# Kernel tuning notes

Hardware: AMD Instinct MI355X
Metric: run time of the kernel (lower is better)

The kernel has to match this reference:

```python
import jax, jax.numpy as jnp
import numpy as np

EPS = 1e-09


def make_spd(x):
    # x: [B1, B2, n, n] random normal -> SPD via Gram matrix + jitter
    n = x.shape[-1]
    g = jnp.einsum('...ik,...jk->...ij', x, x) / n
    return g + 1e-3 * jnp.eye(n, dtype=x.dtype)


def setup_inputs() -> dict:
    key = jax.random.key(0)
    x = jax.random.normal(key, (256, 32, 64, 64), dtype=jnp.float32)
    return {"inputs": make_spd(x)}


def reference(inputs) -> jnp.ndarray:
    # Batched matrix log of SPD matrices: V @ diag(log(relu(w)+eps)) @ V^T
    eigval, eigvecs = jnp.linalg.eigh(inputs)            # [..., n], [..., n, n]
    log_s = jnp.log(jax.nn.relu(eigval) + EPS)           # [..., n]
    # fused reconstruction: (V * log_s) @ V^T
    return jnp.einsum('...ij,...j,...kj->...ik', eigvecs, log_s, eigvecs)
```

## Files before the change

kernel.cpp:

```cpp
#include <hip/hip_runtime.h>
#include <math.h>

#define NDIM 64
#define PITCH 68
#define MAXSWEEPS 20

__global__ __launch_bounds__(64, 2)
void logeig_jacobi_kernel(const float* __restrict__ in, float* __restrict__ out)
{
    const int b    = blockIdx.x;
    const int lane = threadIdx.x;
    const float* A = in  + (size_t)b * (NDIM * NDIM);
    float*       O = out + (size_t)b * (NDIM * NDIM);

    __shared__ float lds[NDIM * PITCH + NDIM];

    float x[NDIM];
#pragma unroll
    for (int i = 0; i < NDIM; ++i)
        x[i] = A[i * NDIM + lane];

    float alpha = 0.0f;
#pragma unroll
    for (int i = 0; i < NDIM; ++i) alpha = fmaf(x[i], x[i], alpha);

#pragma unroll 1
    for (int sweep = 0; sweep < MAXSWEEPS; ++sweep) {
        float a2 = 0.0f;
#pragma unroll
        for (int i = 0; i < NDIM; ++i) a2 = fmaf(x[i], x[i], a2);
        alpha = a2;

        bool sweep_rot = false;
#pragma unroll 1
        for (int mi = 1; mi < NDIM; ++mi) {
            const int m    = (sweep & 1) ? (NDIM - mi) : mi;
            const int pidx = (lane ^ m) << 2;

            float y[NDIM];
#pragma unroll
            for (int i = 0; i < NDIM; ++i)
                y[i] = __int_as_float(__builtin_amdgcn_ds_bpermute(pidx, __float_as_int(x[i])));

            float gamma = 0.0f;
#pragma unroll
            for (int i = 0; i < NDIM; ++i) gamma = fmaf(x[i], y[i], gamma);

            const float other = __int_as_float(__builtin_amdgcn_ds_bpermute(pidx, __float_as_int(alpha)));

            const bool  is_p = lane < (lane ^ m);
            const float aa = is_p ? alpha : other;
            const float bb = is_p ? other : alpha;

            const bool big = (gamma * gamma) > (1e-12f * aa * bb);
            if (__ballot(big) != 0ull) sweep_rot = true;

            const bool rot = (gamma != 0.0f);
            float zeta = (bb - aa) / (2.0f * gamma);
            float az   = fabsf(zeta);
            float t    = 1.0f / (az + sqrtf(1.0f + az * az));
            t = (zeta < 0.0f) ? -t : t;
            float cc = 1.0f / sqrtf(1.0f + t * t);
            float ss = t * cc;

            const float sgn = is_p ? -1.0f : 1.0f;
            const float c_r = rot ? cc : 1.0f;
            const float s_r = rot ? sgn * ss : 0.0f;
            const float tg  = rot ? sgn * t * gamma : 0.0f;

#pragma unroll
            for (int i = 0; i < NDIM; ++i)
                x[i] = fmaf(c_r, x[i], s_r * y[i]);
            alpha += tg;
        }
        if (!sweep_rot) break;
    }

    float af = 0.0f;
#pragma unroll
    for (int i = 0; i < NDIM; ++i) af = fmaf(x[i], x[i], af);
    const float lam = sqrtf(af);
    const float w   = logf(lam + 1e-9f) / af;

    float4* row = (float4*)&lds[lane * PITCH];
#pragma unroll
    for (int t4 = 0; t4 < NDIM / 4; ++t4)
        row[t4] = make_float4(x[4 * t4 + 0], x[4 * t4 + 1], x[4 * t4 + 2], x[4 * t4 + 3]);
    lds[NDIM * PITCH + lane] = w;
    __syncthreads();

    float acc[NDIM];
#pragma unroll
    for (int i = 0; i < NDIM; ++i) acc[i] = 0.0f;

#pragma unroll 1
    for (int k = 0; k < NDIM; ++k) {
        const float wk  = lds[NDIM * PITCH + k];
        const float mjk = lds[k * PITCH + lane];
        const float zk  = wk * mjk;
        const float4* rowk = (const float4*)&lds[k * PITCH];
#pragma unroll
        for (int t4 = 0; t4 < NDIM / 4; ++t4) {
            const float4 v = rowk[t4];
            acc[4 * t4 + 0] = fmaf(zk, v.x, acc[4 * t4 + 0]);
            acc[4 * t4 + 1] = fmaf(zk, v.y, acc[4 * t4 + 1]);
            acc[4 * t4 + 2] = fmaf(zk, v.z, acc[4 * t4 + 2]);
            acc[4 * t4 + 3] = fmaf(zk, v.w, acc[4 * t4 + 3]);
        }
    }

#pragma unroll
    for (int i = 0; i < NDIM; ++i)
        O[i * NDIM + lane] = acc[i];
}

extern "C" void kernel_launch(void* const* d_in, const int* in_sizes, int n_in,
                              void* d_out, int out_size, void* d_ws, size_t ws_size,
                              hipStream_t stream)
{
    const float* in  = (const float*)d_in[0];
    float*       out = (float*)d_out;
    const int nmat = out_size / (NDIM * NDIM);
    hipLaunchKernelGGL(logeig_jacobi_kernel, dim3(nmat), dim3(64), 0, stream, in, out);
}
```

Baseline: 5.825 ms.

## Loosen Jacobi convergence, split dot-product accumulators, chunk LDS reconstruction, raise occupancy

Relaxes the off-diagonal convergence threshold so sweeps can terminate earlier, and splits the gamma dot product into four independent accumulators to shorten the dependency chain. It also stages eigenvector rows into a smaller 16-row LDS buffer in chunks to cut shared memory, and raises the launch-bounds occupancy hint. The looser tolerance risks slightly less accurate eigen-decompositions, and the chunking adds extra barriers.

```diff
diff --git a/kernel.cpp b/kernel.cpp
--- a/kernel.cpp
+++ b/kernel.cpp
@@ -3,9 +3,10 @@
 
 #define NDIM 64
 #define PITCH 68
+#define KC 16
 #define MAXSWEEPS 20
 
-__global__ __launch_bounds__(64, 2)
+__global__ __launch_bounds__(64, 3)
 void logeig_jacobi_kernel(const float* __restrict__ in, float* __restrict__ out)
 {
     const int b    = blockIdx.x;
@@ -13,7 +14,8 @@
     const float* A = in  + (size_t)b * (NDIM * NDIM);
     float*       O = out + (size_t)b * (NDIM * NDIM);
 
-    __shared__ float lds[NDIM * PITCH + NDIM];
+    __shared__ float ldsM[KC * PITCH];
+    __shared__ float ldsW[NDIM];
 
     float x[NDIM];
 #pragma unroll
@@ -42,9 +44,15 @@
             for (int i = 0; i < NDIM; ++i)
                 y[i] = __int_as_float(__builtin_amdgcn_ds_bpermute(pidx, __float_as_int(x[i])));
 
-            float gamma = 0.0f;
+            float g0 = 0.f, g1 = 0.f, g2 = 0.f, g3 = 0.f;
 #pragma unroll
-            for (int i = 0; i < NDIM; ++i) gamma = fmaf(x[i], y[i], gamma);
+            for (int i = 0; i < NDIM; i += 4) {
+                g0 = fmaf(x[i + 0], y[i + 0], g0);
+                g1 = fmaf(x[i + 1], y[i + 1], g1);
+                g2 = fmaf(x[i + 2], y[i + 2], g2);
+                g3 = fmaf(x[i + 3], y[i + 3], g3);
+            }
+            const float gamma = (g0 + g1) + (g2 + g3);
 
             const float other = __int_as_float(__builtin_amdgcn_ds_bpermute(pidx, __float_as_int(alpha)));
 
@@ -52,7 +60,7 @@
             const float aa = is_p ? alpha : other;
             const float bb = is_p ? other : alpha;
 
-            const bool big = (gamma * gamma) > (1e-12f * aa * bb);
+            const bool big = (gamma * gamma) > (1e-9f * aa * bb);
             if (__ballot(big) != 0ull) sweep_rot = true;
 
             const bool rot = (gamma != 0.0f);
@@ -80,32 +88,36 @@
 #pragma unroll
     for (int i = 0; i < NDIM; ++i) af = fmaf(x[i], x[i], af);
     const float lam = sqrtf(af);
-    const float w   = logf(lam + 1e-9f) / af;
-
-    float4* row = (float4*)&lds[lane * PITCH];
-#pragma unroll
-    for (int t4 = 0; t4 < NDIM / 4; ++t4)
-        row[t4] = make_float4(x[4 * t4 + 0], x[4 * t4 + 1], x[4 * t4 + 2], x[4 * t4 + 3]);
-    lds[NDIM * PITCH + lane] = w;
-    __syncthreads();
+    ldsW[lane] = logf(lam + 1e-9f) / af;
 
     float acc[NDIM];
 #pragma unroll
     for (int i = 0; i < NDIM; ++i) acc[i] = 0.0f;
 
 #pragma unroll 1
-    for (int k = 0; k < NDIM; ++k) {
-        const float wk  = lds[NDIM * PITCH + k];
-        const float mjk = lds[k * PITCH + lane];
-        const float zk  = wk * mjk;
-        const float4* rowk = (const float4*)&lds[k * PITCH];
+    for (int c = 0; c < NDIM; c += KC) {
+        __syncthreads();
+        if (lane >= c && lane < c + KC) {
+            float4* row = (float4*)&ldsM[(lane - c) * PITCH];
 #pragma unroll
-        for (int t4 = 0; t4 < NDIM / 4; ++t4) {
-            const float4 v = rowk[t4];
-            acc[4 * t4 + 0] = fmaf(zk, v.x, acc[4 * t4 + 0]);
-            acc[4 * t4 + 1] = fmaf(zk, v.y, acc[4 * t4 + 1]);
-            acc[4 * t4 + 2] = fmaf(zk, v.z, acc[4 * t4 + 2]);
-            acc[4 * t4 + 3] = fmaf(zk, v.w, acc[4 * t4 + 3]);
+            for (int t4 = 0; t4 < NDIM / 4; ++t4)
+                row[t4] = make_float4(x[4 * t4 + 0], x[4 * t4 + 1], x[4 * t4 + 2], x[4 * t4 + 3]);
+        }
+        __syncthreads();
+#pragma unroll 1
+        for (int kk = 0; kk < KC; ++kk) {
+            const float wk  = ldsW[c + kk];
+            const float mlk = ldsM[kk * PITCH + lane];
+            const float zk  = wk * mlk;
+            const float4* rowk = (const float4*)&ldsM[kk * PITCH];
+#pragma unroll
+            for (int t4 = 0; t4 < NDIM / 4; ++t4) {
+                const float4 v = rowk[t4];
+                acc[4 * t4 + 0] = fmaf(zk, v.x, acc[4 * t4 + 0]);
+                acc[4 * t4 + 1] = fmaf(zk, v.y, acc[4 * t4 + 1]);
+                acc[4 * t4 + 2] = fmaf(zk, v.z, acc[4 * t4 + 2]);
+                acc[4 * t4 + 3] = fmaf(zk, v.w, acc[4 * t4 + 3]);
+            }
         }
     }
 
```

Measured after the change: 5.772 ms. Within noise of the previous version (-0.9%).
